# Kernel tuning notes

Hardware: AMD Instinct MI355X
Metric: run time of the kernel (lower is better)

The kernel has to match this reference:

```python
import math
import jax, jax.numpy as jnp
import numpy as np

N_HEAD = 16
ROPE_BASE = 10000.0


def _rope_tables(T, half, dtype):
    # build_sin_cos(seq_len, dim=head_dim//2): inv freq of length `half`
    pos = jnp.arange(T, dtype=jnp.float32)[:, None]                       # (T,1)
    inv = jnp.exp(jnp.arange(0, 2 * half, 2, dtype=jnp.float32) * (-math.log(ROPE_BASE) / (2 * half)))
    ang = pos * inv                                                        # (T, half)
    return jnp.sin(ang).astype(dtype), jnp.cos(ang).astype(dtype)


def _apply_rope(q, k, sin, cos):
    # q,k: (B,T,H,Dh); sin,cos: (T, Dh//2) -> broadcast over batch and heads
    half = q.shape[-1] // 2
    s = sin[None, :, None, :]
    c = cos[None, :, None, :]
    q1, q2 = q[..., :half], q[..., half:]
    k1, k2 = k[..., :half], k[..., half:]
    q = jnp.concatenate([q1 * c - q2 * s, q2 * c + q1 * s], axis=-1)
    k = jnp.concatenate([k1 * c - k2 * s, k2 * c + k1 * s], axis=-1)
    return q, k


def setup_inputs() -> dict:
    key = jax.random.key(0)
    k1, k2, k3 = jax.random.split(key, 3)
    B, T, C = 2, 2048, 2048
    x = jax.random.normal(k1, (B, T, C), dtype=jnp.float32)
    w_qkv = jax.random.normal(k2, (3 * C, C), dtype=jnp.float32) * (1.0 / math.sqrt(C))
    w_proj = jax.random.normal(k3, (C, C), dtype=jnp.float32) * (1.0 / math.sqrt(C))
    return {"x": x, "w_qkv": w_qkv, "w_proj": w_proj}


def reference(x, w_qkv, w_proj):
    B, T, C = x.shape
    H = N_HEAD
    Dh = C // H
    # fused QKV projection (Linear, no bias): (B,T,3C) -> (B,T,3,H,Dh)
    qkv = jnp.einsum('btc,oc->bto', x, w_qkv).reshape(B, T, 3, H, Dh)
    q, k, v = qkv[:, :, 0], qkv[:, :, 1], qkv[:, :, 2]          # (B,T,H,Dh)
    sin, cos = _rope_tables(T, Dh // 2, x.dtype)
    q, k = _apply_rope(q, k, sin, cos)
    # causal attention, scale 1/sqrt(Dh) (flash default softmax_scale=None)
    scale = 1.0 / math.sqrt(Dh)
    scores = jnp.einsum('bqhd,bkhd->bhqk', q, k) * scale        # (B,H,T,T)
    mask = jnp.tril(jnp.ones((T, T), dtype=bool))
    scores = jnp.where(mask[None, None], scores, jnp.finfo(scores.dtype).min)
    probs = jax.nn.softmax(scores, axis=-1)
    out = jnp.einsum('bhqk,bkhd->bqhd', probs, v)               # (B,T,H,Dh)
    # faithful to original: permute(0,2,1,3) then reshape_as(x)
    out = jnp.transpose(out, (0, 2, 1, 3)).reshape(B, T, C)
    return jnp.einsum('btc,oc->bto', out, w_proj)
```

## Files before the change

kernel.cpp:

```cpp
#include <hip/hip_runtime.h>
#include <hip/hip_bf16.h>

typedef __bf16 bf16_t;
typedef __bf16 bf16x8 __attribute__((ext_vector_type(8)));
typedef float f32x4 __attribute__((ext_vector_type(4)));

#define MFMA16(a, b, c) __builtin_amdgcn_mfma_f32_16x16x32_bf16(a, b, c, 0, 0, 0)

__device__ __forceinline__ void async_copy16(const void* g, void* l) {
  __builtin_amdgcn_global_load_lds(
      (const __attribute__((address_space(1))) void*)g,
      (__attribute__((address_space(3))) void*)l, 16, 0, 0);
}

__global__ void cast_f32_bf16(const float* __restrict__ in, bf16_t* __restrict__ out, int n8) {
  int stride = gridDim.x * blockDim.x;
  for (int i = blockIdx.x * blockDim.x + threadIdx.x; i < n8; i += stride) {
    const float* p = in + (size_t)i * 8;
    f32x4 a = *(const f32x4*)p;
    f32x4 b = *(const f32x4*)(p + 4);
    bf16x8 o;
    o[0] = (bf16_t)a[0]; o[1] = (bf16_t)a[1]; o[2] = (bf16_t)a[2]; o[3] = (bf16_t)a[3];
    o[4] = (bf16_t)b[0]; o[5] = (bf16_t)b[1]; o[6] = (bf16_t)b[2]; o[7] = (bf16_t)b[3];
    *(bf16x8*)(out + (size_t)i * 8) = o;
  }
}

__global__ __launch_bounds__(512, 2) void gemm_qkv(
    const bf16_t* __restrict__ A, const bf16_t* __restrict__ Bw,
    bf16_t* __restrict__ qo, bf16_t* __restrict__ ko,
    int K) {
  __shared__ __align__(16) char lds[131072];
  int tid = threadIdx.x;
  int w = tid >> 6, lane = tid & 63;
  int wm = w & 1, wn = w >> 1;
  int mr = lane & 15, kg = lane >> 4;

  int orig = blockIdx.x;
  int chunk = orig & 7, i = orig >> 3;
  int by = (chunk & 3) * 4 + (i & 3);
  int bx = (chunk >> 2) * 8 + (i >> 2);
  int row0 = by * 256, col0 = bx * 256;

  int lr = tid >> 3, ch = (tid & 7) ^ (lr & 7);
  size_t aoff[4], boff[4];
#pragma unroll
  for (int g = 0; g < 4; ++g) {
    int gr = g * 32 + (lr & 31) + (lr >> 5) * 128;
    aoff[g] = (size_t)(row0 + gr) * K + ch * 8;
  }
#pragma unroll
  for (int p = 0; p < 4; ++p) {
    int gr = (lr >> 4) * 64 + p * 16 + (lr & 15);
    boff[p] = (size_t)(col0 + gr) * K + ch * 8;
  }

  auto stgA = [&](int q, int g, int kt) {
    async_copy16(A + aoff[g] + kt * 64, lds + q * 65536 + g * 8192 + tid * 16);
  };
  auto stgB = [&](int q, int p, int kt) {
    async_copy16(Bw + boff[p] + kt * 64, lds + q * 65536 + 32768 + p * 8192 + tid * 16);
  };

  f32x4 zero = {0.f, 0.f, 0.f, 0.f};
  f32x4 acc[8][4];
#pragma unroll
  for (int mi = 0; mi < 8; ++mi)
#pragma unroll
    for (int ni = 0; ni < 4; ++ni) acc[mi][ni] = zero;

  int nt = K >> 6;

  stgB(0, 0, 0); stgB(0, 1, 0); stgB(0, 2, 0); stgB(0, 3, 0);
  stgA(0, 0, 0); stgA(0, 1, 0); stgA(0, 2, 0); stgA(0, 3, 0);
  asm volatile("s_waitcnt vmcnt(0)" ::: "memory");
  __builtin_amdgcn_sched_barrier(0);
  __builtin_amdgcn_s_barrier();
  __builtin_amdgcn_sched_barrier(0);

#pragma unroll 1
  for (int t = 0; t < nt; ++t) {
    int q = t & 1, qn = q ^ 1;
    int kt = (t + 1 < nt) ? (t + 1) : t;
    const char* Ab = lds + q * 65536;
    const char* Bb = Ab + 32768;
    bf16x8 bf[4][2];

#define QKV_PHASE(MI0, STG0, STG1, WAIT)                                        \
    {                                                                           \
      int r0 = ((MI0) >> 1) * 64 + wm * 32 + mr;                                \
      int r1 = r0 + 16;                                                         \
      bf16x8 a00 = *(const bf16x8*)(Ab + r0 * 128 + ((kg * 16) ^ ((r0 & 7) << 4)));      \
      bf16x8 a01 = *(const bf16x8*)(Ab + r0 * 128 + ((64 + kg * 16) ^ ((r0 & 7) << 4))); \
      bf16x8 a10 = *(const bf16x8*)(Ab + r1 * 128 + ((kg * 16) ^ ((r1 & 7) << 4)));      \
      bf16x8 a11 = *(const bf16x8*)(Ab + r1 * 128 + ((64 + kg * 16) ^ ((r1 & 7) << 4))); \
      STG0; STG1;                                                               \
      __builtin_amdgcn_sched_barrier(0);                                        \
      asm volatile("s_waitcnt vmcnt(" #WAIT ")" ::: "memory");                  \
      __builtin_amdgcn_s_barrier();                                             \
      asm volatile("s_waitcnt lgkmcnt(0)" ::: "memory");                        \
      __builtin_amdgcn_sched_barrier(0);                                        \
      __builtin_amdgcn_s_setprio(1);                                            \
      _Pragma("unroll")                                                         \
      for (int ni = 0; ni < 4; ++ni) {                                          \
        acc[MI0][ni] = MFMA16(a00, bf[ni][0], acc[MI0][ni]);                    \
        acc[MI0][ni] = MFMA16(a01, bf[ni][1], acc[MI0][ni]);                    \
        acc[(MI0) + 1][ni] = MFMA16(a10, bf[ni][0], acc[(MI0) + 1][ni]);        \
        acc[(MI0) + 1][ni] = MFMA16(a11, bf[ni][1], acc[(MI0) + 1][ni]);        \
      }                                                                         \
      __builtin_amdgcn_s_setprio(0);                                            \
      __builtin_amdgcn_sched_barrier(0);                                        \
      __builtin_amdgcn_s_barrier();                                             \
      __builtin_amdgcn_sched_barrier(0);                                        \
    }

#pragma unroll
    for (int ni = 0; ni < 4; ++ni) {
      int rb = ni * 64 + wn * 16 + mr;
      bf[ni][0] = *(const bf16x8*)(Bb + rb * 128 + ((kg * 16) ^ ((rb & 7) << 4)));
      bf[ni][1] = *(const bf16x8*)(Bb + rb * 128 + ((64 + kg * 16) ^ ((rb & 7) << 4)));
    }
    QKV_PHASE(0, stgB(qn, 0, kt), stgB(qn, 1, kt), 4)
    QKV_PHASE(2, stgB(qn, 2, kt), stgB(qn, 3, kt), 5)
    QKV_PHASE(4, stgA(qn, 0, kt), stgA(qn, 1, kt), 6)
    QKV_PHASE(6, stgA(qn, 2, kt), stgA(qn, 3, kt), 3)
#undef QKV_PHASE
  }
  asm volatile("s_waitcnt vmcnt(0)" ::: "memory");
  __syncthreads();

  char* tb = &lds[0];
  int s = col0 >> 11;
  int h0 = (col0 >> 7) & 15;
  int b = row0 >> 11, t0 = row0 & 2047;
#pragma unroll
  for (int mi = 0; mi < 8; ++mi)
#pragma unroll
    for (int ni = 0; ni < 4; ++ni)
#pragma unroll
      for (int jj = 0; jj < 4; ++jj) {
        int rl = wm * 128 + mi * 16 + kg * 4 + jj;
        int cb = (wn * 64 + ni * 16 + mr) * 2;
        *(bf16_t*)(tb + rl * 512 + (cb ^ ((rl & 7) << 4))) = (bf16_t)acc[mi][ni][jj];
      }
  __syncthreads();
  int r = tid >> 1, hs = tid & 1;
  const char* rowb = tb + r * 512;
  int sz = (r & 7) << 4;
  int t = t0 + r;
  bf16_t* dst = (s == 0 ? qo : ko) + ((size_t)((b * 16 + h0 + hs) * 2048 + t)) * 128;
  float tf = (float)t;
  const float cinv = -0.20762050593046014f;
  float postm = (s == 0) ? 0.12751744f : 1.0f;
  bf16x8 vin[16];
#pragma unroll
  for (int m = 0; m < 16; ++m)
    vin[m] = *(const bf16x8*)(rowb + ((hs * 256 + m * 16) ^ sz));
#pragma unroll
  for (int m = 0; m < 8; ++m) {
    bf16x8 o1, o2;
#pragma unroll
    for (int e = 0; e < 8; ++e) {
      float ang = tf * exp2f((float)(m * 8 + e) * cinv);
      float sv = __sinf(ang), cv = __cosf(ang);
      float x1 = (float)vin[m][e], x2 = (float)vin[m + 8][e];
      o1[e] = (bf16_t)((x1 * cv - x2 * sv) * postm);
      o2[e] = (bf16_t)((x2 * cv + x1 * sv) * postm);
    }
    *(bf16x8*)(dst + m * 8) = o1;
    *(bf16x8*)(dst + 64 + m * 8) = o2;
  }
}

template <int MODE>
__global__ __launch_bounds__(512, 2) void gemm256(
    const bf16_t* __restrict__ A, const bf16_t* __restrict__ Bw, float* __restrict__ C,
    bf16_t* __restrict__ vto, int M, int N, int K, int nby, int colbase) {
  __shared__ __align__(16) char lds[147456];
  int tid = threadIdx.x;
  int w = tid >> 6, lane = tid & 63;
  int wm = w >> 1, wn = w & 1;
  int mr = lane & 15, kg = lane >> 4;

  int nwg = gridDim.x;
  int orig = blockIdx.x;
  int wgid = (orig & 7) * (nwg >> 3) + (orig >> 3);
  int by = wgid % nby, bx = wgid / nby;
  int row0 = by * 256, col0 = colbase + bx * 128;

  size_t aoff[4], boff[2];
#pragma unroll
  for (int it = 0; it < 4; ++it) {
    int c = tid + it * 512;
    int r = c >> 3;
    int chs = (c & 7) ^ (r & 7);
    aoff[it] = (size_t)(row0 + r) * K + chs * 8;
  }
#pragma unroll
  for (int it = 0; it < 2; ++it) {
    int c = tid + it * 512;
    int r = c >> 3;
    int chs = (c & 7) ^ (r & 7);
    boff[it] = (size_t)(col0 - colbase + r) * K + chs * 8;
  }

  auto stageA = [&](int buf, int kt, int half) {
    char* Ad = &lds[buf * 49152];
#pragma unroll
    for (int it = half * 2; it < half * 2 + 2; ++it)
      async_copy16(A + aoff[it] + kt * 64, Ad + (tid + it * 512) * 16);
  };
  auto stageB = [&](int buf, int kt) {
    char* Bd = &lds[buf * 49152 + 32768];
#pragma unroll
    for (int it = 0; it < 2; ++it)
      async_copy16(Bw + boff[it] + kt * 64, Bd + (tid + it * 512) * 16);
  };

  f32x4 zero = {0.f, 0.f, 0.f, 0.f};
  f32x4 acc[4][4];
#pragma unroll
  for (int mi = 0; mi < 4; ++mi)
#pragma unroll
    for (int ni = 0; ni < 4; ++ni) acc[mi][ni] = zero;

  int nt = K >> 6;
  stageA(0, 0, 0); stageA(0, 0, 1); stageB(0, 0);
  stageA(1, 1, 0); stageA(1, 1, 1); stageB(1, 1);
  asm volatile("s_waitcnt vmcnt(6)" ::: "memory");
  __builtin_amdgcn_sched_barrier(0);
  __builtin_amdgcn_s_barrier();
  __builtin_amdgcn_sched_barrier(0);

#pragma unroll 1
  for (int t = 0; t < nt; ++t) {
    int cur = t % 3;
    int nxt = (t + 2) % 3;
    int kt2 = (t + 2 < nt) ? (t + 2) : t;
    const char* Ab = &lds[cur * 49152];
    const char* Bb = &lds[cur * 49152 + 32768];
    bf16x8 af[4][2], bfr[4][2];
#pragma unroll
    for (int mi = 0; mi < 4; ++mi) {
      int row = wm * 64 + mi * 16 + mr;
      const char* rb = Ab + row * 128;
      int sz = (row & 7) << 4;
      af[mi][0] = *(const bf16x8*)(rb + ((kg * 16) ^ sz));
      af[mi][1] = *(const bf16x8*)(rb + ((64 + kg * 16) ^ sz));
    }
#pragma unroll
    for (int ni = 0; ni < 4; ++ni) {
      int row = wn * 64 + ni * 16 + mr;
      const char* rb = Bb + row * 128;
      int sz = (row & 7) << 4;
      bfr[ni][0] = *(const bf16x8*)(rb + ((kg * 16) ^ sz));
      bfr[ni][1] = *(const bf16x8*)(rb + ((64 + kg * 16) ^ sz));
    }
    stageA(nxt, kt2, 0);
    __builtin_amdgcn_s_setprio(1);
#pragma unroll
    for (int mi = 0; mi < 4; ++mi) {
      acc[mi][0] = MFMA16(af[mi][0], bfr[0][0], acc[mi][0]);
      acc[mi][0] = MFMA16(af[mi][1], bfr[0][1], acc[mi][0]);
    }
    __builtin_amdgcn_s_setprio(0);
    stageA(nxt, kt2, 1);
    __builtin_amdgcn_s_setprio(1);
#pragma unroll
    for (int mi = 0; mi < 4; ++mi) {
      acc[mi][1] = MFMA16(af[mi][0], bfr[1][0], acc[mi][1]);
      acc[mi][1] = MFMA16(af[mi][1], bfr[1][1], acc[mi][1]);
    }
    __builtin_amdgcn_s_setprio(0);
    stageB(nxt, kt2);
    __builtin_amdgcn_s_setprio(1);
#pragma unroll
    for (int mi = 0; mi < 4; ++mi) {
      acc[mi][2] = MFMA16(af[mi][0], bfr[2][0], acc[mi][2]);
      acc[mi][2] = MFMA16(af[mi][1], bfr[2][1], acc[mi][2]);
      acc[mi][3] = MFMA16(af[mi][0], bfr[3][0], acc[mi][3]);
      acc[mi][3] = MFMA16(af[mi][1], bfr[3][1], acc[mi][3]);
    }
    __builtin_amdgcn_s_setprio(0);
    asm volatile("s_waitcnt vmcnt(6)" ::: "memory");
    __builtin_amdgcn_sched_barrier(0);
    __builtin_amdgcn_s_barrier();
    __builtin_amdgcn_sched_barrier(0);
  }
  asm volatile("s_waitcnt vmcnt(0)" ::: "memory");
  __syncthreads();

  if (MODE == 0) {
#pragma unroll
    for (int mi = 0; mi < 4; ++mi)
#pragma unroll
      for (int ni = 0; ni < 4; ++ni)
#pragma unroll
        for (int jj = 0; jj < 4; ++jj) {
          int row = row0 + wm * 64 + mi * 16 + kg * 4 + jj;
          int col = col0 + wn * 64 + ni * 16 + mr;
          C[(size_t)row * N + col] = acc[mi][ni][jj];
        }
  } else {
    char* tb = &lds[0];
    int h = (col0 >> 7) & 15;
    int b = row0 >> 11, t0 = row0 & 2047;
#pragma unroll
    for (int mi = 0; mi < 4; ++mi)
#pragma unroll
      for (int ni = 0; ni < 4; ++ni)
#pragma unroll
        for (int jj = 0; jj < 4; ++jj) {
          int rloc = wm * 64 + mi * 16 + kg * 4 + jj;
          int cloc = wn * 64 + ni * 16 + mr;
          *(bf16_t*)(tb + cloc * 512 + ((rloc * 2) ^ ((cloc & 7) << 4))) =
              (bf16_t)acc[mi][ni][jj];
        }
    __syncthreads();
    int d = tid >> 2, qt = tid & 3;
    const char* rowb = tb + d * 512;
    int sz = (d & 7) << 4;
    bf16_t* dst = vto + ((size_t)((b * 16 + h) * 128 + d)) * 2048 + t0 + qt * 64;
#pragma unroll
    for (int m2 = 0; m2 < 8; ++m2)
      *(bf16x8*)(dst + m2 * 8) = *(const bf16x8*)(rowb + ((qt * 128 + m2 * 16) ^ sz));
  }
}

__global__ __launch_bounds__(512, 2) void attn_kernel(
    const bf16_t* __restrict__ qg, const bf16_t* __restrict__ kgl,
    const bf16_t* __restrict__ vtg, bf16_t* __restrict__ og) {
  __shared__ __align__(16) bf16_t Ks[2][64 * 128];
  __shared__ __align__(16) bf16_t Vs[2][128 * 64];
  __shared__ __align__(16) bf16_t plds[8][1024];
  const int T = 2048;
  int tid = threadIdx.x;
  int w = tid >> 6, lane = tid & 63;
  int mr = lane & 15, kg = lane >> 4;
  int swz = (mr & 7) << 4;

  int L = blockIdx.x;
  int role = (L & 7) * 32 + (L >> 3);
  int bx = role & 7, bh = role >> 3;

  const bf16_t* Q = qg + (size_t)bh * T * 128;
  const bf16_t* K = kgl + (size_t)bh * T * 128;
  const bf16_t* Vt = vtg + (size_t)bh * 128 * T;

  size_t ksrc[2], vsrc[2];
#pragma unroll
  for (int it = 0; it < 2; ++it) {
    int c = it * 512 + tid;
    int sb = c * 16;
    int krl = sb >> 8;
    int kc = (sb & 255) ^ ((krl & 7) << 4);
    ksrc[it] = (size_t)krl * 128 + (kc >> 1);
    int vdl = sb >> 7;
    int vc = (sb & 127) ^ ((vdl & 7) << 4);
    vsrc[it] = (size_t)vdl * 2048 + (vc >> 1);
  }

  auto stage = [&](int buf, int kb) {
#pragma unroll
    for (int it = 0; it < 2; ++it)
      async_copy16(K + (size_t)kb * 128 + ksrc[it], &Ks[buf][(it * 512 + tid) * 8]);
#pragma unroll
    for (int it = 0; it < 2; ++it)
      async_copy16(Vt + kb + vsrc[it], &Vs[buf][(it * 512 + tid) * 8]);
  };

  f32x4 zero = {0.f, 0.f, 0.f, 0.f};
  bf16_t* P = &plds[w][0];
  int b = bh >> 4, h = bh & 15;

#pragma unroll 1
  for (int pp = 0; pp < 2; ++pp) {
    int qb = pp ? bx : (15 - bx);
    int qr0 = qb * 128 + w * 16;
    bf16x8 qf[4];
#pragma unroll
    for (int db = 0; db < 4; ++db)
      qf[db] = *(const bf16x8*)(Q + (size_t)(qr0 + mr) * 128 + db * 32 + kg * 8);

    f32x4 acc[8];
#pragma unroll
    for (int d2 = 0; d2 < 8; ++d2) acc[d2] = zero;
    float mrun[4] = {-1e30f, -1e30f, -1e30f, -1e30f};
    float lpart[4] = {0.f, 0.f, 0.f, 0.f};

    int nj = 2 * qb + 2;
    __syncthreads();
    stage(0, 0);
    if (nj > 1) stage(1, 64);
#pragma unroll 1
    for (int j = 0; j < nj; ++j) {
      int cur = j & 1;
      if (j + 1 < nj) {
        asm volatile("s_waitcnt vmcnt(4)" ::: "memory");
      } else {
        asm volatile("s_waitcnt vmcnt(0)" ::: "memory");
      }
      __builtin_amdgcn_sched_barrier(0);
      __syncthreads();
      const char* KsB = (const char*)&Ks[cur][0];
      const char* VsB = (const char*)&Vs[cur][0];
      int kb = j * 64;
      f32x4 s[4];
      __builtin_amdgcn_s_setprio(1);
#pragma unroll
      for (int ntl = 0; ntl < 4; ++ntl) {
        s[ntl] = zero;
        int rowb = (ntl * 16 + mr) * 256;
#pragma unroll
        for (int db = 0; db < 4; ++db) {
          bf16x8 kf = *(const bf16x8*)(KsB + rowb + ((db * 64 + kg * 16) ^ swz));
          s[ntl] = MFMA16(qf[db], kf, s[ntl]);
        }
      }
      __builtin_amdgcn_s_setprio(0);
      float pvv[4][4];
      float lmax[4] = {-3e38f, -3e38f, -3e38f, -3e38f};
      bool diag = (kb + 63 > qr0);
#pragma unroll
      for (int ntl = 0; ntl < 4; ++ntl)
#pragma unroll
        for (int jj = 0; jj < 4; ++jj) {
          float v = s[ntl][jj];
          if (diag && (kb + ntl * 16 + mr) > (qr0 + kg * 4 + jj)) v = -1e30f;
          pvv[ntl][jj] = v;
          lmax[jj] = fmaxf(lmax[jj], v);
        }
      bool ok = true;
#pragma unroll
      for (int jj = 0; jj < 4; ++jj) ok &= (lmax[jj] <= mrun[jj] + 8.0f);
      if (!__all(ok)) {
        float tmax[4];
#pragma unroll
        for (int jj = 0; jj < 4; ++jj) tmax[jj] = lmax[jj];
#pragma unroll
        for (int m = 1; m < 16; m <<= 1)
#pragma unroll
          for (int jj = 0; jj < 4; ++jj)
            tmax[jj] = fmaxf(tmax[jj], __shfl_xor(tmax[jj], m, 64));
#pragma unroll
        for (int jj = 0; jj < 4; ++jj) {
          float mn = fmaxf(mrun[jj], tmax[jj]);
          float corr = __builtin_amdgcn_exp2f(mrun[jj] - mn);
          mrun[jj] = mn;
          lpart[jj] *= corr;
#pragma unroll
          for (int d2 = 0; d2 < 8; ++d2) acc[d2][jj] *= corr;
        }
      }
#pragma unroll
      for (int ntl = 0; ntl < 4; ++ntl)
#pragma unroll
        for (int jj = 0; jj < 4; ++jj) {
          float p = __builtin_amdgcn_exp2f(pvv[ntl][jj] - mrun[jj]);
          pvv[ntl][jj] = p;
          lpart[jj] += p;
        }
#pragma unroll
      for (int ntl = 0; ntl < 4; ++ntl)
#pragma unroll
        for (int jj = 0; jj < 4; ++jj) {
          int rr = kg * 4 + jj;
          int cbyte = (mr + ntl * 16) * 2;
          *(bf16_t*)((char*)P + rr * 128 + (cbyte ^ ((rr & 7) << 4))) = (bf16_t)pvv[ntl][jj];
        }
      __builtin_amdgcn_s_setprio(1);
#pragma unroll
      for (int ks = 0; ks < 2; ++ks) {
        int cb = (ks * 32 + kg * 8) * 2;
        bf16x8 pa = *(const bf16x8*)((const char*)P + mr * 128 + (cb ^ ((mr & 7) << 4)));
#pragma unroll
        for (int d2 = 0; d2 < 8; ++d2) {
          bf16x8 vf = *(const bf16x8*)(VsB + (d2 * 16 + mr) * 128 + ((ks * 64 + kg * 16) ^ swz));
          acc[d2] = MFMA16(pa, vf, acc[d2]);
        }
      }
      __builtin_amdgcn_s_setprio(0);
      __syncthreads();
      if (j + 2 < nj) stage(cur, (j + 2) * 64);
    }
#pragma unroll
    for (int m = 1; m < 16; m <<= 1)
#pragma unroll
      for (int jj = 0; jj < 4; ++jj) lpart[jj] += __shfl_xor(lpart[jj], m, 64);
#pragma unroll
    for (int jj = 0; jj < 4; ++jj) {
      float invl = 1.0f / lpart[jj];
      int t = qr0 + kg * 4 + jj;
      size_t row = (size_t)b * 2048 + h * 128 + (t >> 4);
      bf16_t* orow = og + row * 2048 + (t & 15) * 128;
#pragma unroll
      for (int d2 = 0; d2 < 8; ++d2)
        orow[d2 * 16 + mr] = (bf16_t)(acc[d2][jj] * invl);
    }
  }
}

extern "C" void kernel_launch(void* const* d_in, const int* in_sizes, int n_in,
                              void* d_out, int out_size, void* d_ws, size_t ws_size,
                              hipStream_t stream) {
  const float* x = (const float*)d_in[0];
  const float* wqkv = (const float*)d_in[1];
  const float* wproj = (const float*)d_in[2];
  float* out = (float*)d_out;
  char* ws = (char*)d_ws;

  const size_t OFF_WQKV = 16777216;
  const size_t OFF_Q = 41943040;
  const size_t OFF_K = 58720256;
  const size_t OFF_VT = 75497472;

  bf16_t* xb = (bf16_t*)(ws);
  bf16_t* wqkvb = (bf16_t*)(ws + OFF_WQKV);
  bf16_t* g_q = (bf16_t*)(ws + OFF_Q);
  bf16_t* g_k = (bf16_t*)(ws + OFF_K);
  bf16_t* g_vt = (bf16_t*)(ws + OFF_VT);
  bf16_t* g_att = (bf16_t*)(ws);
  bf16_t* wprojb = (bf16_t*)(ws + OFF_WQKV);

  cast_f32_bf16<<<2048, 256, 0, stream>>>(x, xb, 8388608 / 8);
  cast_f32_bf16<<<2048, 256, 0, stream>>>(wqkv, wqkvb, 12582912 / 8);
  gemm_qkv<<<256, 512, 0, stream>>>(xb, wqkvb, g_q, g_k, 2048);
  gemm256<1><<<256, 512, 0, stream>>>(xb, wqkvb + (size_t)4096 * 2048, nullptr, g_vt,
                                      4096, 2048, 2048, 16, 4096);
  cast_f32_bf16<<<2048, 256, 0, stream>>>(wproj, wprojb, 4194304 / 8);
  attn_kernel<<<256, 512, 0, stream>>>(g_q, g_k, g_vt, g_att);
  gemm256<0><<<256, 512, 0, stream>>>(g_att, wprojb, out, nullptr, 4096, 2048, 2048, 16, 0);
}
```

Measured before the change: 249.6 us.

## Rewrite attention with 32x32 MFMA, register-resident P, and 4-wave blocks

The attention kernel moves from 16x16x32 MFMA tiles with 8 waves of 16 query rows to 32x32x16 MFMA tiles with 4 waves of 32 query rows each. It computes S^T so the softmax probabilities stay in registers and become the PV operand through packed bf16 conversion and cross-half lane shuffles, replacing the per-wave LDS round trip for P. Waves also skip fully masked key blocks. The trade-off is fewer threads per block, which lowers occupancy and latency hiding, plus higher register pressure from the f32x16 accumulators.

```diff
diff --git a/kernel.cpp b/kernel.cpp
--- a/kernel.cpp
+++ b/kernel.cpp
@@ -3,14 +3,24 @@
 
 typedef __bf16 bf16_t;
 typedef __bf16 bf16x8 __attribute__((ext_vector_type(8)));
+typedef __bf16 bf16x4 __attribute__((ext_vector_type(4)));
 typedef float f32x4 __attribute__((ext_vector_type(4)));
+typedef float f32x16 __attribute__((ext_vector_type(16)));
+typedef unsigned u32x4v __attribute__((ext_vector_type(4)));
 
 #define MFMA16(a, b, c) __builtin_amdgcn_mfma_f32_16x16x32_bf16(a, b, c, 0, 0, 0)
+#define MFMA32(a, b, c) __builtin_amdgcn_mfma_f32_32x32x16_bf16(a, b, c, 0, 0, 0)
 
 __device__ __forceinline__ void async_copy16(const void* g, void* l) {
   __builtin_amdgcn_global_load_lds(
       (const __attribute__((address_space(1))) void*)g,
       (__attribute__((address_space(3))) void*)l, 16, 0, 0);
+}
+
+__device__ __forceinline__ unsigned cvtpk(float lo, float hi) {
+  unsigned r;
+  asm("v_cvt_pk_bf16_f32 %0, %1, %2" : "=v"(r) : "v"(lo), "v"(hi));
+  return r;
 }
 
 __global__ void cast_f32_bf16(const float* __restrict__ in, bf16_t* __restrict__ out, int n8) {
@@ -327,17 +337,15 @@
   }
 }
 
-__global__ __launch_bounds__(512, 2) void attn_kernel(
+__global__ __launch_bounds__(256, 1) void attn_kernel(
     const bf16_t* __restrict__ qg, const bf16_t* __restrict__ kgl,
     const bf16_t* __restrict__ vtg, bf16_t* __restrict__ og) {
   __shared__ __align__(16) bf16_t Ks[2][64 * 128];
   __shared__ __align__(16) bf16_t Vs[2][128 * 64];
-  __shared__ __align__(16) bf16_t plds[8][1024];
   const int T = 2048;
   int tid = threadIdx.x;
   int w = tid >> 6, lane = tid & 63;
-  int mr = lane & 15, kg = lane >> 4;
-  int swz = (mr & 7) << 4;
+  int l31 = lane & 31, hi = lane >> 5;
 
   int L = blockIdx.x;
   int role = (L & 7) * 32 + (L >> 3);
@@ -347,156 +355,156 @@
   const bf16_t* K = kgl + (size_t)bh * T * 128;
   const bf16_t* Vt = vtg + (size_t)bh * 128 * T;
 
-  size_t ksrc[2], vsrc[2];
-#pragma unroll
-  for (int it = 0; it < 2; ++it) {
-    int c = it * 512 + tid;
-    int sb = c * 16;
-    int krl = sb >> 8;
-    int kc = (sb & 255) ^ ((krl & 7) << 4);
-    ksrc[it] = (size_t)krl * 128 + (kc >> 1);
-    int vdl = sb >> 7;
-    int vc = (sb & 127) ^ ((vdl & 7) << 4);
-    vsrc[it] = (size_t)vdl * 2048 + (vc >> 1);
-  }
+  int sb = tid * 16;
+  int krl = sb >> 8;
+  int kc = (sb & 255) ^ (krl << 4);
+  size_t ksrc = (size_t)krl * 128 + (kc >> 1);
+  int vdl = sb >> 7;
+  int vc = (sb & 127) ^ ((vdl & 7) << 4);
+  size_t vsrc = (size_t)vdl * 2048 + (vc >> 1);
 
   auto stage = [&](int buf, int kb) {
 #pragma unroll
-    for (int it = 0; it < 2; ++it)
-      async_copy16(K + (size_t)kb * 128 + ksrc[it], &Ks[buf][(it * 512 + tid) * 8]);
-#pragma unroll
-    for (int it = 0; it < 2; ++it)
-      async_copy16(Vt + kb + vsrc[it], &Vs[buf][(it * 512 + tid) * 8]);
+    for (int it = 0; it < 4; ++it)
+      async_copy16(K + (size_t)(kb + it * 16) * 128 + ksrc, &Ks[buf][it * 2048 + tid * 8]);
+#pragma unroll
+    for (int it = 0; it < 4; ++it)
+      async_copy16(Vt + (size_t)it * 65536 + kb + vsrc, &Vs[buf][it * 2048 + tid * 8]);
   };
 
-  f32x4 zero = {0.f, 0.f, 0.f, 0.f};
-  bf16_t* P = &plds[w][0];
   int b = bh >> 4, h = bh & 15;
+  f32x16 zero16 = {0.f};
+  int swzK = l31 << 4;
+  swzK = (l31 & 15) << 4;
+  int swzV = (l31 & 7) << 4;
 
 #pragma unroll 1
   for (int pp = 0; pp < 2; ++pp) {
     int qb = pp ? bx : (15 - bx);
-    int qr0 = qb * 128 + w * 16;
-    bf16x8 qf[4];
-#pragma unroll
-    for (int db = 0; db < 4; ++db)
-      qf[db] = *(const bf16x8*)(Q + (size_t)(qr0 + mr) * 128 + db * 32 + kg * 8);
-
-    f32x4 acc[8];
-#pragma unroll
-    for (int d2 = 0; d2 < 8; ++d2) acc[d2] = zero;
-    float mrun[4] = {-1e30f, -1e30f, -1e30f, -1e30f};
-    float lpart[4] = {0.f, 0.f, 0.f, 0.f};
+    int qw0 = qb * 128 + w * 32;
+    int tq = qw0 + l31;
+    const bf16_t* qrow = Q + (size_t)tq * 128 + hi * 8;
+    bf16x8 qf[8];
+#pragma unroll
+    for (int dc = 0; dc < 8; ++dc) qf[dc] = *(const bf16x8*)(qrow + dc * 16);
+
+    f32x16 acc[4];
+#pragma unroll
+    for (int dt = 0; dt < 4; ++dt) acc[dt] = zero16;
+    float mrun = -1e30f, lpart = 0.f;
 
     int nj = 2 * qb + 2;
     __syncthreads();
     stage(0, 0);
-    if (nj > 1) stage(1, 64);
+    stage(1, 64);
 #pragma unroll 1
     for (int j = 0; j < nj; ++j) {
       int cur = j & 1;
       if (j + 1 < nj) {
-        asm volatile("s_waitcnt vmcnt(4)" ::: "memory");
+        asm volatile("s_waitcnt vmcnt(8)" ::: "memory");
       } else {
         asm volatile("s_waitcnt vmcnt(0)" ::: "memory");
       }
       __builtin_amdgcn_sched_barrier(0);
       __syncthreads();
-      const char* KsB = (const char*)&Ks[cur][0];
-      const char* VsB = (const char*)&Vs[cur][0];
       int kb = j * 64;
-      f32x4 s[4];
-      __builtin_amdgcn_s_setprio(1);
-#pragma unroll
-      for (int ntl = 0; ntl < 4; ++ntl) {
-        s[ntl] = zero;
-        int rowb = (ntl * 16 + mr) * 256;
-#pragma unroll
-        for (int db = 0; db < 4; ++db) {
-          bf16x8 kf = *(const bf16x8*)(KsB + rowb + ((db * 64 + kg * 16) ^ swz));
-          s[ntl] = MFMA16(qf[db], kf, s[ntl]);
-        }
+      if (kb <= qw0) {
+        const char* KsB = (const char*)&Ks[cur][0];
+        const char* VsB = (const char*)&Vs[cur][0];
+        f32x16 s0 = zero16, s1 = zero16;
+        __builtin_amdgcn_s_setprio(1);
+#pragma unroll
+        for (int dc = 0; dc < 8; ++dc) {
+          int cb = dc * 32 + hi * 16;
+          bf16x8 k0 = *(const bf16x8*)(KsB + l31 * 256 + (cb ^ swzK));
+          bf16x8 k1 = *(const bf16x8*)(KsB + (32 + l31) * 256 + (cb ^ swzK));
+          s0 = MFMA32(k0, qf[dc], s0);
+          s1 = MFMA32(k1, qf[dc], s1);
+        }
+        __builtin_amdgcn_s_setprio(0);
+        float p0[16], p1[16];
+        float lmax = -3e38f;
+        bool diag = (kb + 63 > qw0);
+#pragma unroll
+        for (int r = 0; r < 16; ++r) {
+          int kk = (r & 3) + 8 * (r >> 2) + 4 * hi;
+          float v0 = s0[r], v1 = s1[r];
+          if (diag) {
+            if (kb + kk > tq) v0 = -1e30f;
+            if (kb + 32 + kk > tq) v1 = -1e30f;
+          }
+          p0[r] = v0; p1[r] = v1;
+          lmax = fmaxf(lmax, fmaxf(v0, v1));
+        }
+        bool ok = (lmax <= mrun + 8.0f);
+        if (!__all(ok)) {
+          float tmax = fmaxf(lmax, __shfl_xor(lmax, 32, 64));
+          float mn = fmaxf(mrun, tmax);
+          float corr = __builtin_amdgcn_exp2f(mrun - mn);
+          mrun = mn;
+          lpart *= corr;
+#pragma unroll
+          for (int dt = 0; dt < 4; ++dt)
+#pragma unroll
+            for (int r = 0; r < 16; ++r) acc[dt][r] *= corr;
+        }
+#pragma unroll
+        for (int r = 0; r < 16; ++r) {
+          float e0 = __builtin_amdgcn_exp2f(p0[r] - mrun);
+          float e1 = __builtin_amdgcn_exp2f(p1[r] - mrun);
+          p0[r] = e0; p1[r] = e1;
+          lpart += e0 + e1;
+        }
+        bf16x8 pa0, pa1, pa2, pa3;
+#define BUILD_PA(dst, P, B0)                                         \
+        { unsigned a0 = cvtpk(P[(B0) + 0], P[(B0) + 1]);             \
+          unsigned a1 = cvtpk(P[(B0) + 2], P[(B0) + 3]);             \
+          unsigned b0 = cvtpk(P[(B0) + 4], P[(B0) + 5]);             \
+          unsigned b1 = cvtpk(P[(B0) + 6], P[(B0) + 7]);             \
+          unsigned xa0 = __shfl_xor(a0, 32, 64);                     \
+          unsigned xa1 = __shfl_xor(a1, 32, 64);                     \
+          unsigned xb0 = __shfl_xor(b0, 32, 64);                     \
+          unsigned xb1 = __shfl_xor(b1, 32, 64);                     \
+          u32x4v fw;                                                 \
+          fw[0] = hi ? xb0 : a0; fw[1] = hi ? xb1 : a1;              \
+          fw[2] = hi ? b0 : xa0; fw[3] = hi ? b1 : xa1;              \
+          dst = __builtin_bit_cast(bf16x8, fw); }
+        BUILD_PA(pa0, p0, 0)
+        BUILD_PA(pa1, p0, 8)
+        BUILD_PA(pa2, p1, 0)
+        BUILD_PA(pa3, p1, 8)
+#undef BUILD_PA
+        __builtin_amdgcn_s_setprio(1);
+#pragma unroll
+        for (int dt = 0; dt < 4; ++dt) {
+          const char* vrow = VsB + (dt * 32 + l31) * 128;
+          bf16x8 v0 = *(const bf16x8*)(vrow + ((hi * 16) ^ swzV));
+          bf16x8 v1 = *(const bf16x8*)(vrow + ((32 + hi * 16) ^ swzV));
+          bf16x8 v2 = *(const bf16x8*)(vrow + ((64 + hi * 16) ^ swzV));
+          bf16x8 v3 = *(const bf16x8*)(vrow + ((96 + hi * 16) ^ swzV));
+          acc[dt] = MFMA32(v0, pa0, acc[dt]);
+          acc[dt] = MFMA32(v1, pa1, acc[dt]);
+          acc[dt] = MFMA32(v2, pa2, acc[dt]);
+          acc[dt] = MFMA32(v3, pa3, acc[dt]);
+        }
+        __builtin_amdgcn_s_setprio(0);
       }
-      __builtin_amdgcn_s_setprio(0);
-      float pvv[4][4];
-      float lmax[4] = {-3e38f, -3e38f, -3e38f, -3e38f};
-      bool diag = (kb + 63 > qr0);
-#pragma unroll
-      for (int ntl = 0; ntl < 4; ++ntl)
-#pragma unroll
-        for (int jj = 0; jj < 4; ++jj) {
-          float v = s[ntl][jj];
-          if (diag && (kb + ntl * 16 + mr) > (qr0 + kg * 4 + jj)) v = -1e30f;
-          pvv[ntl][jj] = v;
-          lmax[jj] = fmaxf(lmax[jj], v);
-        }
-      bool ok = true;
-#pragma unroll
-      for (int jj = 0; jj < 4; ++jj) ok &= (lmax[jj] <= mrun[jj] + 8.0f);
-      if (!__all(ok)) {
-        float tmax[4];
-#pragma unroll
-        for (int jj = 0; jj < 4; ++jj) tmax[jj] = lmax[jj];
-#pragma unroll
-        for (int m = 1; m < 16; m <<= 1)
-#pragma unroll
-          for (int jj = 0; jj < 4; ++jj)
-            tmax[jj] = fmaxf(tmax[jj], __shfl_xor(tmax[jj], m, 64));
-#pragma unroll
-        for (int jj = 0; jj < 4; ++jj) {
-          float mn = fmaxf(mrun[jj], tmax[jj]);
-          float corr = __builtin_amdgcn_exp2f(mrun[jj] - mn);
-          mrun[jj] = mn;
-          lpart[jj] *= corr;
-#pragma unroll
-          for (int d2 = 0; d2 < 8; ++d2) acc[d2][jj] *= corr;
-        }
-      }
-#pragma unroll
-      for (int ntl = 0; ntl < 4; ++ntl)
-#pragma unroll
-        for (int jj = 0; jj < 4; ++jj) {
-          float p = __builtin_amdgcn_exp2f(pvv[ntl][jj] - mrun[jj]);
-          pvv[ntl][jj] = p;
-          lpart[jj] += p;
-        }
-#pragma unroll
-      for (int ntl = 0; ntl < 4; ++ntl)
-#pragma unroll
-        for (int jj = 0; jj < 4; ++jj) {
-          int rr = kg * 4 + jj;
-          int cbyte = (mr + ntl * 16) * 2;
-          *(bf16_t*)((char*)P + rr * 128 + (cbyte ^ ((rr & 7) << 4))) = (bf16_t)pvv[ntl][jj];
-        }
-      __builtin_amdgcn_s_setprio(1);
-#pragma unroll
-      for (int ks = 0; ks < 2; ++ks) {
-        int cb = (ks * 32 + kg * 8) * 2;
-        bf16x8 pa = *(const bf16x8*)((const char*)P + mr * 128 + (cb ^ ((mr & 7) << 4)));
-#pragma unroll
-        for (int d2 = 0; d2 < 8; ++d2) {
-          bf16x8 vf = *(const bf16x8*)(VsB + (d2 * 16 + mr) * 128 + ((ks * 64 + kg * 16) ^ swz));
-          acc[d2] = MFMA16(pa, vf, acc[d2]);
-        }
-      }
-      __builtin_amdgcn_s_setprio(0);
       __syncthreads();
       if (j + 2 < nj) stage(cur, (j + 2) * 64);
     }
-#pragma unroll
-    for (int m = 1; m < 16; m <<= 1)
-#pragma unroll
-      for (int jj = 0; jj < 4; ++jj) lpart[jj] += __shfl_xor(lpart[jj], m, 64);
-#pragma unroll
-    for (int jj = 0; jj < 4; ++jj) {
-      float invl = 1.0f / lpart[jj];
-      int t = qr0 + kg * 4 + jj;
-      size_t row = (size_t)b * 2048 + h * 128 + (t >> 4);
-      bf16_t* orow = og + row * 2048 + (t & 15) * 128;
-#pragma unroll
-      for (int d2 = 0; d2 < 8; ++d2)
-        orow[d2 * 16 + mr] = (bf16_t)(acc[d2][jj] * invl);
-    }
+    float l = lpart + __shfl_xor(lpart, 32, 64);
+    float invl = 1.0f / l;
+    size_t orow_idx = (size_t)b * 2048 + h * 128 + (tq >> 4);
+    bf16_t* orow = og + orow_idx * 2048 + (tq & 15) * 128;
+#pragma unroll
+    for (int dt = 0; dt < 4; ++dt)
+#pragma unroll
+      for (int g = 0; g < 4; ++g) {
+        bf16x4 v4;
+#pragma unroll
+        for (int e = 0; e < 4; ++e) v4[e] = (bf16_t)(acc[dt][4 * g + e] * invl);
+        *(bf16x4*)(orow + dt * 32 + 8 * g + 4 * hi) = v4;
+      }
   }
 }
 
@@ -528,6 +536,6 @@
   gemm256<1><<<256, 512, 0, stream>>>(xb, wqkvb + (size_t)4096 * 2048, nullptr, g_vt,
                                       4096, 2048, 2048, 16, 4096);
   cast_f32_bf16<<<2048, 256, 0, stream>>>(wproj, wprojb, 4194304 / 8);
-  attn_kernel<<<256, 512, 0, stream>>>(g_q, g_k, g_vt, g_att);
+  attn_kernel<<<256, 256, 0, stream>>>(g_q, g_k, g_vt, g_att);
   gemm256<0><<<256, 512, 0, stream>>>(g_att, wprojb, out, nullptr, 4096, 2048, 2048, 16, 0);
 }
```

Measured after the change: 251.0 us. About the same (+0.6%).
